# Kernel tuning notes

Hardware: AMD Instinct MI355X
Metric: run time of the kernel (lower is better)

## Reference

```python
import jax, jax.numpy as jnp
import numpy as np

B, S, D, H, DK, DV, DFF, V, L = 2, 1024, 768, 12, 64, 64, 3072, 32000, 4
PAD_ID = 0


def _pos_enc(seq_len, dim):
    # sinusoidal PE: pe[:,0::2]=sin(pos/scale), pe[:,1::2]=cos(pos/scale)
    pos = jnp.arange(seq_len, dtype=jnp.float32)[:, None]
    idx = jnp.arange(dim // 2, dtype=jnp.float32)
    scale = 10000.0 ** (2.0 * idx / dim)
    ang = pos / scale  # [S, D/2]
    return jnp.stack([jnp.sin(ang), jnp.cos(ang)], axis=-1).reshape(seq_len, dim)


def _layernorm(x, s, b):
    m = jnp.mean(x, axis=-1, keepdims=True)
    v = jnp.var(x, axis=-1, keepdims=True)
    return (x - m) / jnp.sqrt(v + 1e-5) * s + b


def setup_inputs() -> dict:
    key = jax.random.key(0)
    ks = jax.random.split(key, 12)
    emb = jax.random.normal(ks[0], (V, D), jnp.float32) * 0.02
    emb = emb.at[PAD_ID].set(0.0)  # padding_idx row zeroed (nn.Embedding padding_idx)
    inp = {
        'x': jax.random.randint(ks[1], (B, S), 0, V),
        'emb': emb,
        'Wq': jax.random.normal(ks[2], (L, D, H * DK), jnp.float32) * 0.02,
        'Wk': jax.random.normal(ks[3], (L, D, H * DK), jnp.float32) * 0.02,
        'Wv': jax.random.normal(ks[4], (L, D, H * DV), jnp.float32) * 0.02,
        'Wo': jax.random.normal(ks[5], (L, H * DV, D), jnp.float32) * 0.02,
        'ln1_s': jnp.ones((L, D), jnp.float32),
        'ln1_b': jnp.zeros((L, D), jnp.float32),
        'W1': jax.random.normal(ks[6], (L, D, DFF), jnp.float32) * 0.02,
        'b1': jnp.zeros((L, DFF), jnp.float32),
        'W2': jax.random.normal(ks[7], (L, DFF, D), jnp.float32) * 0.02,
        'b2': jnp.zeros((L, D), jnp.float32),
        'ln2_s': jnp.ones((L, D), jnp.float32),
        'ln2_b': jnp.zeros((L, D), jnp.float32),
        'lm_W': jax.random.normal(ks[8], (D, V), jnp.float32) * 0.02,
        'lm_b': jnp.zeros((V,), jnp.float32),
    }
    return inp


def reference(x, emb, Wq, Wk, Wv, Wo, ln1_s, ln1_b, W1, b1, W2, b2, ln2_s, ln2_b, lm_W, lm_b):
    Bx, Sx = x.shape
    h = emb[x] + _pos_enc(Sx, D)  # [B, S, D]
    # causal mask from torch.triu(ones, diagonal=0): True on diagonal and above
    # (each token is prevented from attending to itself and future tokens)
    mask = jnp.triu(jnp.ones((Sx, Sx), dtype=bool))
    inv_sqrt_dk = 1.0 / jnp.sqrt(jnp.float32(DK))
    for l in range(L):
        q = (h @ Wq[l]).reshape(Bx, Sx, H, DK).transpose(0, 2, 1, 3)
        k = (h @ Wk[l]).reshape(Bx, Sx, H, DK).transpose(0, 2, 1, 3)
        v = (h @ Wv[l]).reshape(Bx, Sx, H, DV).transpose(0, 2, 1, 3)
        scores = jnp.einsum('bhqd,bhkd->bhqk', q, k) * inv_sqrt_dk
        scores = jnp.where(mask, -jnp.inf, scores)
        # source's custom _stable_softmax: exp(x) / (sum(exp(x)) + 1e-9)
        e = jnp.exp(scores)
        w = e / (jnp.sum(e, axis=-1, keepdims=True) + 1e-9)
        av = jnp.einsum('bhqk,bhkd->bhqd', w, v)
        av = av.transpose(0, 2, 1, 3).reshape(Bx, Sx, H * DV)
        h = _layernorm(h + av @ Wo[l], ln1_s[l], ln1_b[l])
        ff = jax.nn.gelu(h @ W1[l] + b1[l], approximate=False) @ W2[l] + b2[l]
        h = _layernorm(h + ff, ln2_s[l], ln2_b[l])
    return h @ lm_W + lm_b  # [B, S, V] logits
```

## Files before the change

kernel.cpp:

```cpp
#include <hip/hip_runtime.h>
#include <hip/hip_bf16.h>

#define L_LAYERS 4
#define D_MODEL 768
#define SEQ 1024
#define BATCH 2
#define NHEAD 12
#define HDIM 64
#define DFF_DIM 3072
#define VOCAB 32000
#define MROWS (BATCH*SEQ)
#define QKV_PLANE (NHEAD*BATCH*SEQ*HDIM)

typedef __attribute__((ext_vector_type(8))) short bfrag8;
typedef __attribute__((ext_vector_type(4))) float facc4;

#define EPI_PLAIN 0
#define EPI_BIAS 1
#define EPI_GELU_BF16 2
#define EPI_QKV 3

__device__ __forceinline__ void gld_lds16(const __hip_bfloat16* g, __hip_bfloat16* l) {
    __builtin_amdgcn_global_load_lds((const __attribute__((address_space(1))) void*)g,
                                     (__attribute__((address_space(3))) void*)l, 16, 0, 0);
}

__global__ __launch_bounds__(256) void transpose_cast(
    const float* __restrict__ src, __hip_bfloat16* __restrict__ dst,
    const int K, const int N, const long sL, const long dL)
{
    __shared__ float tile[32][33];
    const int z = blockIdx.z;
    const float* s = src + (long)z * sL;
    __hip_bfloat16* d = dst + (long)z * dL;
    const int bx = blockIdx.x * 32;
    const int by = blockIdx.y * 32;
    const int tx = threadIdx.x, ty = threadIdx.y;
    #pragma unroll
    for (int r = 0; r < 4; ++r)
        tile[ty + r*8][tx] = s[(long)(by + ty + r*8) * N + bx + tx];
    __syncthreads();
    #pragma unroll
    for (int r = 0; r < 4; ++r)
        d[(long)(bx + ty + r*8) * K + by + tx] = __float2bfloat16(tile[tx][ty + r*8]);
}

__global__ __launch_bounds__(256) void embed_k(
    const int* __restrict__ xids, const float* __restrict__ emb,
    float* __restrict__ h, __hip_bfloat16* __restrict__ hb)
{
    const int row = blockIdx.x, t = threadIdx.x;
    const int tok = xids[row];
    const int spos = row & (SEQ - 1);
    const long base = (long)row * D_MODEL;
    const long ebase = (long)tok * D_MODEL;
    #pragma unroll
    for (int j = 0; j < 3; ++j) {
        const int d = j*256 + t;
        const int i = d >> 1;
        const float ang = (float)spos * expf(-(float)(2*i) * (9.210340371976184f / 768.0f));
        const float pe = (d & 1) ? cosf(ang) : sinf(ang);
        const float v = emb[ebase + d] + pe;
        h[base + d] = v;
        hb[base + d] = __float2bfloat16(v);
    }
}

__global__ __launch_bounds__(256) void ln_residual(
    float* __restrict__ h, __hip_bfloat16* __restrict__ hb,
    const float* __restrict__ delta,
    const float* __restrict__ sc, const float* __restrict__ bi,
    const int nplanes)
{
    const int row = blockIdx.x, t = threadIdx.x;
    const long base = (long)row * D_MODEL;
    float x[3];
    float s1 = 0.f, s2 = 0.f;
    #pragma unroll
    for (int j = 0; j < 3; ++j) {
        const int d = j*256 + t;
        float v = h[base + d];
        for (int p = 0; p < nplanes; ++p)
            v += delta[(long)p * MROWS * D_MODEL + base + d];
        x[j] = v; s1 += v; s2 += v*v;
    }
    #pragma unroll
    for (int off = 32; off >= 1; off >>= 1) {
        s1 += __shfl_xor(s1, off);
        s2 += __shfl_xor(s2, off);
    }
    __shared__ float r1[4], r2[4];
    const int wv = t >> 6;
    if ((t & 63) == 0) { r1[wv] = s1; r2[wv] = s2; }
    __syncthreads();
    s1 = r1[0] + r1[1] + r1[2] + r1[3];
    s2 = r2[0] + r2[1] + r2[2] + r2[3];
    const float mean = s1 * (1.0f/768.0f);
    const float var  = s2 * (1.0f/768.0f) - mean*mean;
    const float inv  = rsqrtf(var + 1e-5f);
    #pragma unroll
    for (int j = 0; j < 3; ++j) {
        const int d = j*256 + t;
        const float y = (x[j] - mean) * inv * sc[d] + bi[d];
        h[base + d] = y;
        hb[base + d] = __float2bfloat16(y);
    }
}

__global__ __launch_bounds__(256) void gemm_bt(
    const __hip_bfloat16* __restrict__ A,
    const __hip_bfloat16* __restrict__ Bt,
    const float* __restrict__ bias,
    float* __restrict__ outf,
    __hip_bfloat16* __restrict__ outb,
    const int N, const int K, const int epi)
{
    __shared__ __hip_bfloat16 As[2][128*32];
    __shared__ __hip_bfloat16 Bs[2][128*32];
    const int tid = threadIdx.x;
    const int lane = tid & 63, wv = tid >> 6;

    const int nwg  = gridDim.x * gridDim.y;
    const int orig = blockIdx.y * gridDim.x + blockIdx.x;
    const int qq = nwg >> 3, rr = nwg & 7;
    const int xcd = orig & 7, lin = orig >> 3;
    const int wgid = (xcd < rr ? xcd * (qq + 1) : rr * (qq + 1) + (xcd - rr) * qq) + lin;
    const int m8   = wgid & 7;
    const int rest = wgid >> 3;
    const int bni  = rest % gridDim.x;
    const int bmi  = (rest / gridDim.x) * 8 + m8;
    const int bm = bmi * 128, bn = bni * 128;

    const int wm = (wv >> 1) * 64, wn = (wv & 1) * 64;
    const int fr = lane & 15, fq = lane >> 4;

    const int Kc = K / gridDim.z;
    const long zoff = (long)blockIdx.z * Kc;

    facc4 acc[4][4];
    #pragma unroll
    for (int i = 0; i < 4; ++i)
        #pragma unroll
        for (int j = 0; j < 4; ++j) { facc4 z = {0.f,0.f,0.f,0.f}; acc[i][j] = z; }

    const int srow = wv*32 + (lane >> 2);
    const int scol = (lane & 3) * 8;
    const __hip_bfloat16* Ag = A  + (long)(bm + srow) * K + scol + zoff;
    const __hip_bfloat16* Bg = Bt + (long)(bn + srow) * K + scol + zoff;
    __hip_bfloat16* Aw0 = &As[0][wv*1024];
    __hip_bfloat16* Aw1 = &As[1][wv*1024];
    __hip_bfloat16* Bw0 = &Bs[0][wv*1024];
    __hip_bfloat16* Bw1 = &Bs[1][wv*1024];

    const int nt = Kc >> 5;
    gld_lds16(Ag,                 Aw0);
    gld_lds16(Ag + (long)16*K,    Aw0 + 512);
    gld_lds16(Bg,                 Bw0);
    gld_lds16(Bg + (long)16*K,    Bw0 + 512);

    int cur = 0;
    for (int t = 0; t < nt; ++t) {
        __syncthreads();
        if (t + 1 < nt) {
            const int k0 = (t + 1) << 5;
            __hip_bfloat16* aw = cur ? Aw0 : Aw1;
            __hip_bfloat16* bw = cur ? Bw0 : Bw1;
            gld_lds16(Ag + k0,              aw);
            gld_lds16(Ag + k0 + (long)16*K, aw + 512);
            gld_lds16(Bg + k0,              bw);
            gld_lds16(Bg + k0 + (long)16*K, bw + 512);
        }
        const __hip_bfloat16* Ab = cur ? &As[1][0] : &As[0][0];
        const __hip_bfloat16* Bb = cur ? &Bs[1][0] : &Bs[0][0];
        bfrag8 af[4], bf[4];
        #pragma unroll
        for (int i = 0; i < 4; ++i) af[i] = *(const bfrag8*)(Ab + (wm + i*16 + fr)*32 + fq*8);
        #pragma unroll
        for (int j = 0; j < 4; ++j) bf[j] = *(const bfrag8*)(Bb + (wn + j*16 + fr)*32 + fq*8);
        #pragma unroll
        for (int i = 0; i < 4; ++i)
            #pragma unroll
            for (int j = 0; j < 4; ++j)
                acc[i][j] = __builtin_amdgcn_mfma_f32_16x16x32_bf16(af[i], bf[j], acc[i][j], 0, 0, 0);
        cur ^= 1;
    }

    if (epi == EPI_QKV) {
        __hip_bfloat16* qo = outb;
        __hip_bfloat16* ko = outb + QKV_PLANE;
        __hip_bfloat16* vo = outb + 2*QKV_PLANE;
        #pragma unroll
        for (int i = 0; i < 4; ++i) {
            #pragma unroll
            for (int j = 0; j < 4; ++j) {
                const int gn = bn + wn + j*16 + fr;
                const int which = gn / D_MODEL;
                const int nn = gn - which * D_MODEL;
                const int hh = nn >> 6, dd = nn & 63;
                #pragma unroll
                for (int r = 0; r < 4; ++r) {
                    const int gm = bm + wm + i*16 + fq*4 + r;
                    const int bidx = gm >> 10, si = gm & (SEQ-1);
                    const long bh = (long)bidx * NHEAD + hh;
                    const __hip_bfloat16 bv = __float2bfloat16(acc[i][j][r]);
                    if (which == 0)      qo[(bh*SEQ + si)*HDIM + dd] = bv;
                    else if (which == 1) ko[(bh*SEQ + si)*HDIM + dd] = bv;
                    else                 vo[(bh*HDIM + dd)*SEQ + si] = bv;
                }
            }
        }
    } else if (epi == EPI_GELU_BF16) {
        #pragma unroll
        for (int i = 0; i < 4; ++i)
            #pragma unroll
            for (int j = 0; j < 4; ++j) {
                const int gn = bn + wn + j*16 + fr;
                const float bb = bias[gn];
                #pragma unroll
                for (int r = 0; r < 4; ++r) {
                    const int gm = bm + wm + i*16 + fq*4 + r;
                    const float v = acc[i][j][r] + bb;
                    const float g = 0.5f * v * (1.0f + erff(v * 0.70710678118f));
                    outb[(long)gm * N + gn] = __float2bfloat16(g);
                }
            }
    } else if (epi == EPI_BIAS) {
        float* outz = outf + (long)blockIdx.z * (long)(gridDim.y * 128) * N;
        #pragma unroll
        for (int i = 0; i < 4; ++i)
            #pragma unroll
            for (int j = 0; j < 4; ++j) {
                const int gn = bn + wn + j*16 + fr;
                const float bb = (blockIdx.z == 0) ? bias[gn] : 0.f;
                #pragma unroll
                for (int r = 0; r < 4; ++r) {
                    const int gm = bm + wm + i*16 + fq*4 + r;
                    outz[(long)gm * N + gn] = acc[i][j][r] + bb;
                }
            }
    } else {
        float* outz = outf + (long)blockIdx.z * (long)(gridDim.y * 128) * N;
        #pragma unroll
        for (int i = 0; i < 4; ++i)
            #pragma unroll
            for (int j = 0; j < 4; ++j) {
                const int gn = bn + wn + j*16 + fr;
                #pragma unroll
                for (int r = 0; r < 4; ++r) {
                    const int gm = bm + wm + i*16 + fq*4 + r;
                    outz[(long)gm * N + gn] = acc[i][j][r];
                }
            }
    }
}

#define KS_STRIDE 80
#define VS_STRIDE 40
#define PS_STRIDE 40
__global__ __launch_bounds__(256) void attn_flash(
    const __hip_bfloat16* __restrict__ Q,
    const __hip_bfloat16* __restrict__ Kp,
    const __hip_bfloat16* __restrict__ Vt,
    __hip_bfloat16* __restrict__ avo)
{
    __shared__ __hip_bfloat16 Ks[32*KS_STRIDE];
    __shared__ __hip_bfloat16 Vs[64*VS_STRIDE];
    __shared__ __hip_bfloat16 Ps[4][16*PS_STRIDE];
    const int tid = threadIdx.x;
    const int lane = tid & 63, wv = tid >> 6;
    const int fr = lane & 15, fq = lane >> 4;
    const int q0 = blockIdx.x * 64;
    const int bh = blockIdx.y;
    const int qrow = q0 + wv*16;

    const __hip_bfloat16* qp = Q + ((long)bh*SEQ + qrow + fr)*HDIM + fq*8;
    const bfrag8 aq0 = *(const bfrag8*)(qp);
    const bfrag8 aq1 = *(const bfrag8*)(qp + 32);

    facc4 accv[4];
    #pragma unroll
    for (int n = 0; n < 4; ++n) { facc4 z = {0.f,0.f,0.f,0.f}; accv[n] = z; }
    float denom[4] = {0.f, 0.f, 0.f, 0.f};

    const __hip_bfloat16* kg = Kp + ((long)bh*SEQ + (tid>>3))*HDIM + (tid&7)*8;
    const __hip_bfloat16* vg = Vt + ((long)bh*HDIM + (tid>>2))*SEQ + (tid&3)*8;
    __hip_bfloat16* ksw = Ks + (tid>>3)*KS_STRIDE + (tid&7)*8;
    __hip_bfloat16* vsw = Vs + (tid>>2)*VS_STRIDE + (tid&3)*8;

    bfrag8 kr = *(const bfrag8*)(kg);
    bfrag8 vr = *(const bfrag8*)(vg);

    const int kend = q0 + 64;
    for (int k0 = 0; k0 < kend; k0 += 32) {
        __syncthreads();
        *(bfrag8*)ksw = kr;
        *(bfrag8*)vsw = vr;
        const long knext = (k0 + 32 < kend) ? (long)(k0 + 32) : (long)k0;
        kr = *(const bfrag8*)(kg + knext * HDIM);
        vr = *(const bfrag8*)(vg + knext);
        __syncthreads();
        #pragma unroll
        for (int t = 0; t < 2; ++t) {
            const int koff = t*16;
            const bfrag8 bk0 = *(const bfrag8*)(Ks + (koff + fr)*KS_STRIDE + fq*8);
            const bfrag8 bk1 = *(const bfrag8*)(Ks + (koff + fr)*KS_STRIDE + 32 + fq*8);
            facc4 sc = {0.f,0.f,0.f,0.f};
            __builtin_amdgcn_s_setprio(1);
            sc = __builtin_amdgcn_mfma_f32_16x16x32_bf16(aq0, bk0, sc, 0, 0, 0);
            sc = __builtin_amdgcn_mfma_f32_16x16x32_bf16(aq1, bk1, sc, 0, 0, 0);
            __builtin_amdgcn_s_setprio(0);
            const int ki = k0 + koff + fr;
            #pragma unroll
            for (int r = 0; r < 4; ++r) {
                const int qi = qrow + fq*4 + r;
                const float e = (ki < qi) ? __expf(sc[r] * 0.125f) : 0.f;
                denom[r] += e;
                Ps[wv][(fq*4 + r)*PS_STRIDE + koff + fr] = __float2bfloat16(e);
            }
        }
        asm volatile("s_waitcnt lgkmcnt(0)" ::: "memory");
        __builtin_amdgcn_sched_barrier(0);
        const bfrag8 ap = *(const bfrag8*)(&Ps[wv][fr*PS_STRIDE + fq*8]);
        __builtin_amdgcn_s_setprio(1);
        #pragma unroll
        for (int n = 0; n < 4; ++n) {
            const bfrag8 bv = *(const bfrag8*)(Vs + (n*16 + fr)*VS_STRIDE + fq*8);
            accv[n] = __builtin_amdgcn_mfma_f32_16x16x32_bf16(ap, bv, accv[n], 0, 0, 0);
        }
        __builtin_amdgcn_s_setprio(0);
    }

    #pragma unroll
    for (int r = 0; r < 4; ++r) {
        #pragma unroll
        for (int off = 1; off < 16; off <<= 1) denom[r] += __shfl_xor(denom[r], off);
    }
    const int bidx = bh / NHEAD, hh = bh % NHEAD;
    #pragma unroll
    for (int n = 0; n < 4; ++n) {
        #pragma unroll
        for (int r = 0; r < 4; ++r) {
            const int qi = qrow + fq*4 + r;
            const int dd = n*16 + fr;
            const float o = accv[n][r] / (denom[r] + 1e-9f);
            avo[((long)(bidx*SEQ + qi))*D_MODEL + hh*HDIM + dd] = __float2bfloat16(o);
        }
    }
}

extern "C" void kernel_launch(void* const* d_in, const int* in_sizes, int n_in,
                              void* d_out, int out_size, void* d_ws, size_t ws_size,
                              hipStream_t stream) {
    const int*   x    = (const int*)d_in[0];
    const float* emb  = (const float*)d_in[1];
    const float* Wq   = (const float*)d_in[2];
    const float* Wk   = (const float*)d_in[3];
    const float* Wv   = (const float*)d_in[4];
    const float* Wo   = (const float*)d_in[5];
    const float* ln1s = (const float*)d_in[6];
    const float* ln1b = (const float*)d_in[7];
    const float* W1   = (const float*)d_in[8];
    const float* b1   = (const float*)d_in[9];
    const float* W2   = (const float*)d_in[10];
    const float* b2   = (const float*)d_in[11];
    const float* ln2s = (const float*)d_in[12];
    const float* ln2b = (const float*)d_in[13];
    const float* lmW  = (const float*)d_in[14];
    const float* lmb  = (const float*)d_in[15];
    float* out = (float*)d_out;

    char* wsp = (char*)d_ws;
    size_t off = 0;
    auto take = [&](size_t bytes) -> char* {
        char* p = wsp + off;
        off += (bytes + 255) & ~(size_t)255;
        return p;
    };
    __hip_bfloat16* wqkvT = (__hip_bfloat16*)take((size_t)L_LAYERS*2304*768*2);
    __hip_bfloat16* woT   = (__hip_bfloat16*)take((size_t)L_LAYERS*768*768*2);
    __hip_bfloat16* w1T   = (__hip_bfloat16*)take((size_t)L_LAYERS*3072*768*2);
    __hip_bfloat16* w2T   = (__hip_bfloat16*)take((size_t)L_LAYERS*768*3072*2);
    __hip_bfloat16* lmT   = (__hip_bfloat16*)take((size_t)VOCAB*768*2);
    float*          hbuf  = (float*)take((size_t)MROWS*D_MODEL*4);
    __hip_bfloat16* hb    = (__hip_bfloat16*)take((size_t)MROWS*D_MODEL*2);
    __hip_bfloat16* qkvb  = (__hip_bfloat16*)take((size_t)3*QKV_PLANE*2);
    __hip_bfloat16* avb   = (__hip_bfloat16*)take((size_t)MROWS*D_MODEL*2);
    __hip_bfloat16* ffb   = (__hip_bfloat16*)take((size_t)MROWS*DFF_DIM*2);
    float*          tmp   = (float*)take((size_t)4*MROWS*D_MODEL*4);

    dim3 tb(32, 8);
    transpose_cast<<<dim3(24,24,4), tb, 0, stream>>>(Wq, wqkvT,              768, 768, (long)768*768, (long)2304*768);
    transpose_cast<<<dim3(24,24,4), tb, 0, stream>>>(Wk, wqkvT + 768*768,    768, 768, (long)768*768, (long)2304*768);
    transpose_cast<<<dim3(24,24,4), tb, 0, stream>>>(Wv, wqkvT + 2*768*768,  768, 768, (long)768*768, (long)2304*768);
    transpose_cast<<<dim3(24,24,4), tb, 0, stream>>>(Wo, woT,                768, 768, (long)768*768, (long)768*768);
    transpose_cast<<<dim3(96,24,4), tb, 0, stream>>>(W1, w1T,                768, 3072, (long)768*3072, (long)3072*768);
    transpose_cast<<<dim3(24,96,4), tb, 0, stream>>>(W2, w2T,                3072, 768, (long)3072*768, (long)768*3072);
    transpose_cast<<<dim3(1000,24,1), tb, 0, stream>>>(lmW, lmT,             768, VOCAB, 0, 0);

    embed_k<<<MROWS, 256, 0, stream>>>(x, emb, hbuf, hb);

    for (int l = 0; l < L_LAYERS; ++l) {
        gemm_bt<<<dim3(18,16), 256, 0, stream>>>(hb, wqkvT + (size_t)l*2304*768, nullptr,
                                                 nullptr, qkvb, 2304, 768, EPI_QKV);
        attn_flash<<<dim3(16,24), 256, 0, stream>>>(qkvb, qkvb + QKV_PLANE, qkvb + 2*QKV_PLANE, avb);
        gemm_bt<<<dim3(6,16,2), 256, 0, stream>>>(avb, woT + (size_t)l*768*768, nullptr,
                                                  tmp, nullptr, 768, 768, EPI_PLAIN);
        ln_residual<<<MROWS, 256, 0, stream>>>(hbuf, hb, tmp, ln1s + l*768, ln1b + l*768, 2);
        gemm_bt<<<dim3(24,16), 256, 0, stream>>>(hb, w1T + (size_t)l*3072*768, b1 + l*DFF_DIM,
                                                 nullptr, ffb, DFF_DIM, 768, EPI_GELU_BF16);
        gemm_bt<<<dim3(6,16,4), 256, 0, stream>>>(ffb, w2T + (size_t)l*768*3072, b2 + l*768,
                                                  tmp, nullptr, 768, DFF_DIM, EPI_BIAS);
        ln_residual<<<MROWS, 256, 0, stream>>>(hbuf, hb, tmp, ln2s + l*768, ln2b + l*768, 4);
    }
    gemm_bt<<<dim3(250,16), 256, 0, stream>>>(hb, lmT, lmb, out, nullptr, VOCAB, 768, EPI_BIAS);
}
```

Before: 1.164 ms.

## Add 256x256 tiled double-buffered GEMM kernel for the LM head projection

```diff
diff --git a/kernel.cpp b/kernel.cpp
--- a/kernel.cpp
+++ b/kernel.cpp
@@ -251,6 +251,136 @@
                     outz[(long)gm * N + gn] = acc[i][j][r];
                 }
             }
+    }
+}
+
+__global__ __launch_bounds__(512, 2) void gemm256_bias(
+    const __hip_bfloat16* __restrict__ A,
+    const __hip_bfloat16* __restrict__ Bt,
+    const float* __restrict__ bias,
+    float* __restrict__ outf,
+    const int N, const int K)
+{
+    __shared__ __hip_bfloat16 ldsA[2][16384];
+    __shared__ __hip_bfloat16 ldsB[2][16384];
+
+    const int tid = threadIdx.x;
+    const int lane = tid & 63, wv = tid >> 6;
+    const int fr = lane & 15, fq = (lane >> 4) & 3;
+    const int wr = wv >> 2, wc = wv & 3;
+
+    const int nwg  = gridDim.x;
+    const int cpx  = nwg >> 3;
+    const int orig = blockIdx.x;
+    const int wgid = (orig & 7) * cpx + (orig >> 3);
+    const int bm = (wgid & 7) * 256;
+    const int bn = (wgid >> 3) * 256;
+
+    const int trow = tid >> 3;
+    const int sg   = (tid & 7) ^ (trow & 7);
+    const __hip_bfloat16* Ag = A  + (long)(bm + trow) * K + sg * 8;
+    const __hip_bfloat16* Bg = Bt + (long)(bn + trow) * K + sg * 8;
+
+#define STAGE_PAIR(m, kt1, buf) do { \
+    gld_lds16(Ag + (long)((m)*64) * K + (kt1)*64, &ldsA[buf][(m)*4096 + wv*512]); \
+    gld_lds16(Bg + (long)((m)*64) * K + (kt1)*64, &ldsB[buf][(m)*4096 + wv*512]); \
+  } while (0)
+
+    facc4 acc[8][4];
+    #pragma unroll
+    for (int i = 0; i < 8; ++i)
+        #pragma unroll
+        for (int j = 0; j < 4; ++j) { facc4 z = {0.f,0.f,0.f,0.f}; acc[i][j] = z; }
+
+    const int rowA = wr * 128 + fr;
+    const int rowB = wc * 64  + fr;
+    const int sx0 = ((fq)     ^ (fr & 7)) * 8;
+    const int sx1 = ((4 + fq) ^ (fr & 7)) * 8;
+
+    const int nt = K >> 6;
+    STAGE_PAIR(0, 0, 0); STAGE_PAIR(1, 0, 0); STAGE_PAIR(2, 0, 0); STAGE_PAIR(3, 0, 0);
+
+    for (int kt = 0; kt < nt; ++kt) {
+        const int p = kt & 1;
+        const __hip_bfloat16* Ac = ldsA[p];
+        const __hip_bfloat16* Bc = ldsB[p];
+        const bool pre = (kt + 1 < nt);
+
+        if (pre) {
+            STAGE_PAIR(0, kt+1, p^1);
+            asm volatile("s_waitcnt vmcnt(2)" ::: "memory");
+        } else {
+            asm volatile("s_waitcnt vmcnt(0)" ::: "memory");
+        }
+        __builtin_amdgcn_s_barrier();
+        bfrag8 b[4][2];
+        #pragma unroll
+        for (int j = 0; j < 4; ++j) {
+            b[j][0] = *(const bfrag8*)(Bc + (rowB + j*16)*64 + sx0);
+            b[j][1] = *(const bfrag8*)(Bc + (rowB + j*16)*64 + sx1);
+        }
+        {
+            bfrag8 a[2][2];
+            #pragma unroll
+            for (int ii = 0; ii < 2; ++ii) {
+                a[ii][0] = *(const bfrag8*)(Ac + (rowA + ii*16)*64 + sx0);
+                a[ii][1] = *(const bfrag8*)(Ac + (rowA + ii*16)*64 + sx1);
+            }
+            asm volatile("s_waitcnt lgkmcnt(0)" ::: "memory");
+            __builtin_amdgcn_sched_barrier(0);
+            __builtin_amdgcn_s_setprio(1);
+            #pragma unroll
+            for (int jj = 0; jj < 4; ++jj)
+                #pragma unroll
+                for (int ii = 0; ii < 2; ++ii) {
+                    acc[ii][jj] = __builtin_amdgcn_mfma_f32_16x16x32_bf16(a[ii][0], b[jj][0], acc[ii][jj], 0, 0, 0);
+                    acc[ii][jj] = __builtin_amdgcn_mfma_f32_16x16x32_bf16(a[ii][1], b[jj][1], acc[ii][jj], 0, 0, 0);
+                }
+            __builtin_amdgcn_s_setprio(0);
+        }
+        __builtin_amdgcn_s_barrier();
+
+        #pragma unroll
+        for (int q = 1; q < 4; ++q) {
+            bfrag8 a[2][2];
+            #pragma unroll
+            for (int ii = 0; ii < 2; ++ii) {
+                a[ii][0] = *(const bfrag8*)(Ac + (rowA + (q*2+ii)*16)*64 + sx0);
+                a[ii][1] = *(const bfrag8*)(Ac + (rowA + (q*2+ii)*16)*64 + sx1);
+            }
+            if (pre) {
+                if (q == 1)      STAGE_PAIR(1, kt+1, p^1);
+                else if (q == 2) STAGE_PAIR(2, kt+1, p^1);
+                else             STAGE_PAIR(3, kt+1, p^1);
+            }
+            __builtin_amdgcn_s_barrier();
+            asm volatile("s_waitcnt lgkmcnt(0)" ::: "memory");
+            __builtin_amdgcn_sched_barrier(0);
+            __builtin_amdgcn_s_setprio(1);
+            #pragma unroll
+            for (int jj = 0; jj < 4; ++jj)
+                #pragma unroll
+                for (int ii = 0; ii < 2; ++ii) {
+                    acc[q*2+ii][jj] = __builtin_amdgcn_mfma_f32_16x16x32_bf16(a[ii][0], b[jj][0], acc[q*2+ii][jj], 0, 0, 0);
+                    acc[q*2+ii][jj] = __builtin_amdgcn_mfma_f32_16x16x32_bf16(a[ii][1], b[jj][1], acc[q*2+ii][jj], 0, 0, 0);
+                }
+            __builtin_amdgcn_s_setprio(0);
+            __builtin_amdgcn_s_barrier();
+        }
+    }
+#undef STAGE_PAIR
+
+    #pragma unroll
+    for (int i = 0; i < 8; ++i) {
+        const int gm = bm + wr*128 + i*16 + fq*4;
+        #pragma unroll
+        for (int j = 0; j < 4; ++j) {
+            const int gn = bn + wc*64 + j*16 + fr;
+            const float bb = bias[gn];
+            #pragma unroll
+            for (int rr = 0; rr < 4; ++rr)
+                outf[(long)(gm + rr) * N + gn] = acc[i][j][rr] + bb;
+        }
     }
 }
 
@@ -412,5 +542,5 @@
                                                   tmp, nullptr, 768, DFF_DIM, EPI_BIAS);
         ln_residual<<<MROWS, 256, 0, stream>>>(hbuf, hb, tmp, ln2s + l*768, ln2b + l*768, 4);
     }
-    gemm_bt<<<dim3(250,16), 256, 0, stream>>>(hb, lmT, lmb, out, nullptr, VOCAB, 768, EPI_BIAS);
-}
+    gemm256_bias<<<1000, 512, 0, stream>>>(hb, lmT, lmb, out, VOCAB, 768);
+}
```

Result: no change. 1.161 ms (-0.2%).
